# Kernel optimization log

Hardware: AMD Instinct MI355X
Metric: run time of the kernel (lower is better)

## Reference

```python
import jax, jax.numpy as jnp
import numpy as np

EXP_EMBD = 1024
EXP_Q_H = 8
EXP_HEAD_DIM = 256
EXP_KV_H = 1
EXP_KV_DIM = EXP_KV_H * EXP_HEAD_DIM  # 256
EXP_FFN = 4096
B, L, LC = 8, 512, 2048


def setup_inputs() -> dict:
    key = jax.random.key(0)
    ks = jax.random.split(key, 12)
    def w(k, shape):
        fan_in = shape[-1]
        return jax.random.normal(k, shape, jnp.float32) * (fan_in ** -0.5)
    return {
        "x": jax.random.normal(ks[0], (B, L, EXP_EMBD), jnp.float32),
        "text_k": jax.random.normal(ks[1], (B, LC, EXP_KV_DIM), jnp.float32),
        "text_v": jax.random.normal(ks[2], (B, LC, EXP_KV_DIM), jnp.float32),
        "ln1_w": jnp.ones((EXP_EMBD,), jnp.float32),
        "ln2_w": jnp.ones((EXP_EMBD,), jnp.float32),
        "Wq": w(ks[3], (EXP_Q_H * EXP_HEAD_DIM, EXP_EMBD)),
        "Wk": w(ks[4], (EXP_KV_DIM, EXP_KV_DIM)),
        "Wv": w(ks[5], (EXP_KV_DIM, EXP_KV_DIM)),
        "Wo": w(ks[6], (EXP_EMBD, EXP_Q_H * EXP_HEAD_DIM)),
        "Wg": w(ks[7], (EXP_FFN, EXP_EMBD)),
        "Wu": w(ks[8], (EXP_FFN, EXP_EMBD)),
        "Wd": w(ks[9], (EXP_EMBD, EXP_FFN)),
    }


def _rmsnorm(x, w):
    # torch.nn.RMSNorm with eps=None -> eps = finfo(dtype).eps
    eps = jnp.asarray(jnp.finfo(jnp.float32).eps, x.dtype)
    return x * jax.lax.rsqrt(jnp.mean(x * x, axis=-1, keepdims=True) + eps) * w


def _rope(x):
    # x: [B, L, H, D]
    b, l, h, d = x.shape
    d2 = d // 2
    ts = 10000.0 ** (2.0 / d * jnp.arange(d2, dtype=jnp.float32))  # [d2]
    rad = jnp.arange(l, dtype=jnp.float32)[:, None] / ts[None, :]  # [L, d2]
    s = jnp.sin(rad)[None, :, None, :]
    c = jnp.cos(rad)[None, :, None, :]
    x1, x2 = x[..., :d2], x[..., d2:]
    return jnp.concatenate([x1 * c - x2 * s, x2 * c + x1 * s], axis=-1)


def reference(x, text_k, text_v, ln1_w, ln2_w, Wq, Wk, Wv, Wo, Wg, Wu, Wd):
    b, l, _ = x.shape
    lc = text_k.shape[1]
    residual = x
    h = _rmsnorm(x, ln1_w)
    q = _rope((h @ Wq.T).reshape(b, l, EXP_Q_H, EXP_HEAD_DIM))          # [B,L,QH,D]
    k = (text_k @ Wk.T).reshape(b, lc, EXP_KV_H, EXP_HEAD_DIM)          # [B,Lc,KVH,D]
    v = (text_v @ Wv.T).reshape(b, lc, EXP_KV_H, EXP_HEAD_DIM)
    kv_map = (jnp.arange(EXP_Q_H) * EXP_KV_H) // EXP_Q_H                # GQA head map
    kh = jnp.take(k, kv_map, axis=2)                                    # [B,Lc,QH,D]
    vh = jnp.take(v, kv_map, axis=2)
    scale = 1.0 / np.sqrt(EXP_HEAD_DIM).astype(np.float32)
    scores = jnp.einsum('blhd,bchd->bhlc', q, kh) * scale               # [B,QH,L,Lc]
    attn = jax.nn.softmax(scores, axis=-1)
    ctx = jnp.einsum('bhlc,bchd->blhd', attn, vh).reshape(b, l, -1)
    x = ctx @ Wo.T + residual
    residual = x
    h = _rmsnorm(x, ln2_w)
    return (jax.nn.silu(h @ Wg.T) * (h @ Wu.T)) @ Wd.T + residual
```

## Files before the change

kernel.cpp:

```cpp
#include <hip/hip_runtime.h>

typedef __attribute__((ext_vector_type(4))) float f32x4;
typedef __attribute__((ext_vector_type(8))) short s16x8;
typedef __attribute__((ext_vector_type(4))) unsigned short u16x4;

#define B_    8
#define L_    512
#define LC_   2048
#define EMBD  1024

__device__ __forceinline__ float b2f(unsigned short u) {
  unsigned int i = ((unsigned int)u) << 16;
  float f; __builtin_memcpy(&f, &i, 4); return f;
}
__device__ __forceinline__ unsigned short f2b(float f) {
  unsigned int i; __builtin_memcpy(&i, &f, 4);
  unsigned int r = i + 0x7FFFu + ((i >> 16) & 1u);
  return (unsigned short)(r >> 16);
}

#define GLL16(g, l)                                                         \
  __builtin_amdgcn_global_load_lds(                                         \
      (__attribute__((address_space(1))) void*)(g),                         \
      (__attribute__((address_space(3))) void*)(l), 16, 0, 0)

__global__ __launch_bounds__(256) void convert_f32_bf16(
    const float* __restrict__ in, unsigned short* __restrict__ out, int n4) {
  int i = blockIdx.x * 256 + threadIdx.x;
  if (i >= n4) return;
  float4 v = ((const float4*)in)[i];
  u16x4 o = { f2b(v.x), f2b(v.y), f2b(v.z), f2b(v.w) };
  ((u16x4*)out)[i] = o;
}

__global__ __launch_bounds__(256) void rmsnorm_kernel(
    const float* __restrict__ x, const float* __restrict__ w,
    unsigned short* __restrict__ out) {
  int row = blockIdx.x;
  int tid = threadIdx.x;
  float4 v = ((const float4*)(x + (size_t)row * EMBD))[tid];
  float ss = v.x*v.x + v.y*v.y + v.z*v.z + v.w*v.w;
#pragma unroll
  for (int o = 1; o < 64; o <<= 1) ss += __shfl_xor(ss, o);
  __shared__ float red[4];
  if ((tid & 63) == 0) red[tid >> 6] = ss;
  __syncthreads();
  float tot = red[0] + red[1] + red[2] + red[3];
  float rs = rsqrtf(tot * (1.0f / EMBD) + 1.1920928955078125e-07f);
  float4 wv = ((const float4*)w)[tid];
  u16x4 o = { f2b(v.x*rs*wv.x), f2b(v.y*rs*wv.y), f2b(v.z*rs*wv.z), f2b(v.w*rs*wv.w) };
  ((u16x4*)(out + (size_t)row * EMBD))[tid] = o;
}

__global__ __launch_bounds__(256) void rope_kernel(unsigned short* __restrict__ q) {
  int idx = blockIdx.x * 256 + threadIdx.x;
  int i   = idx & 127;
  int h   = (idx >> 7) & 7;
  int row = idx >> 10;
  int l   = row & (L_ - 1);
  size_t base = (size_t)row * 2048 + h * 256 + i;
  float x1 = b2f(q[base]);
  float x2 = b2f(q[base + 128]);
  float ts  = powf(10000.0f, (float)i * (2.0f / 256.0f));
  float rad = (float)l / ts;
  float s, c;
  sincosf(rad, &s, &c);
  q[base]       = f2b(x1 * c - x2 * s);
  q[base + 128] = f2b(x2 * c + x1 * s);
}

__global__ __launch_bounds__(256) void act_kernel(
    const unsigned short* __restrict__ g, const unsigned short* __restrict__ u,
    unsigned short* __restrict__ out, int n8) {
  int i = blockIdx.x * 256 + threadIdx.x;
  if (i >= n8) return;
  s16x8 gv = ((const s16x8*)g)[i];
  s16x8 uv = ((const s16x8*)u)[i];
  s16x8 ov;
#pragma unroll
  for (int j = 0; j < 8; ++j) {
    float gf = b2f((unsigned short)gv[j]);
    float uf = b2f((unsigned short)uv[j]);
    float s  = gf / (1.0f + __expf(-gf));
    ov[j] = (short)f2b(s * uf);
  }
  ((s16x8*)out)[i] = ov;
}

template <int ADD_RES, int OUT_BF16>
__global__ __launch_bounds__(256, 2) void gemm_nt(
    const unsigned short* __restrict__ A, const unsigned short* __restrict__ Bw,
    const float* __restrict__ Res, void* __restrict__ C, int M, int N, int K) {
  __shared__ unsigned short As[128 * 64];
  __shared__ unsigned short Bs[128 * 64];
  const int tid = threadIdx.x;
  const int lane = tid & 63, wid = tid >> 6;
  const int l15 = lane & 15, l4 = lane >> 4;
  const int wr = wid >> 1, wc = wid & 1;
  const int m0 = blockIdx.y * 128, n0 = blockIdx.x * 128;

  const f32x4 fz = {0.f, 0.f, 0.f, 0.f};
  f32x4 acc[4][4];
#pragma unroll
  for (int i = 0; i < 4; ++i)
#pragma unroll
    for (int j = 0; j < 4; ++j) acc[i][j] = fz;

  for (int k0 = 0; k0 < K; k0 += 64) {
    __syncthreads();
#pragma unroll
    for (int i = 0; i < 4; ++i) {
      int Li = i * 4096 + tid * 16;
      int row = Li >> 7;
      int kb = (Li & 127) ^ ((row & 7) << 4);
      GLL16((const char*)(A + (size_t)(m0 + row) * K + k0) + kb, (char*)As + Li);
      GLL16((const char*)(Bw + (size_t)(n0 + row) * K + k0) + kb, (char*)Bs + Li);
    }
    __syncthreads();
#pragma unroll
    for (int kk = 0; kk < 2; ++kk) {
      s16x8 af[4], bfr[4];
#pragma unroll
      for (int mi = 0; mi < 4; ++mi) {
        int row = wr * 64 + mi * 16 + l15;
        int kb = (kk * 64 + l4 * 16) ^ ((row & 7) << 4);
        af[mi] = *(const s16x8*)((const char*)As + row * 128 + kb);
      }
#pragma unroll
      for (int ni = 0; ni < 4; ++ni) {
        int row = wc * 64 + ni * 16 + l15;
        int kb = (kk * 64 + l4 * 16) ^ ((row & 7) << 4);
        bfr[ni] = *(const s16x8*)((const char*)Bs + row * 128 + kb);
      }
#pragma unroll
      for (int mi = 0; mi < 4; ++mi)
#pragma unroll
        for (int ni = 0; ni < 4; ++ni)
          acc[mi][ni] = __builtin_amdgcn_mfma_f32_16x16x32_bf16(
              af[mi], bfr[ni], acc[mi][ni], 0, 0, 0);
    }
  }
#pragma unroll
  for (int mi = 0; mi < 4; ++mi) {
#pragma unroll
    for (int r = 0; r < 4; ++r) {
      int grow = m0 + wr * 64 + mi * 16 + l4 * 4 + r;
      size_t base = (size_t)grow * N + n0 + wc * 64 + l15;
#pragma unroll
      for (int ni = 0; ni < 4; ++ni) {
        float v = acc[mi][ni][r];
        size_t idx = base + ni * 16;
        if (ADD_RES) v += Res[idx];
        if (OUT_BF16) ((unsigned short*)C)[idx] = f2b(v);
        else          ((float*)C)[idx] = v;
      }
    }
  }
}

#define SWZV(d) (((((d) & 7) ^ (((d) >> 3) & 7))) << 4)

__global__ __launch_bounds__(512, 2) void attn_kernel(
    const unsigned short* __restrict__ Q,
    const unsigned short* __restrict__ Kc,
    const unsigned short* __restrict__ Vc,
    unsigned short* __restrict__ Ctx) {
  __shared__ unsigned short Ks[64 * 256];
  __shared__ unsigned short Vt[256 * 64];
  const int tid = threadIdx.x;
  const int lane = tid & 63, wid = tid >> 6;
  const int l15 = lane & 15, g = lane >> 4;
  const int qt = blockIdx.x, h = blockIdx.y, b = blockIdx.z;

  const size_t qrow = (size_t)(b * L_ + qt * 128 + wid * 16 + l15);
  const unsigned short* qp = Q + qrow * 2048 + h * 256;
  s16x8 qf[8];
#pragma unroll
  for (int kc = 0; kc < 8; ++kc) qf[kc] = *(const s16x8*)(qp + kc * 32 + g * 8);

  const f32x4 fz = {0.f, 0.f, 0.f, 0.f};
  f32x4 oacc[16];
#pragma unroll
  for (int i = 0; i < 16; ++i) oacc[i] = fz;
  float m_run = -__builtin_inff(), l_run = 0.f;

  const unsigned short* Kb = Kc + (size_t)b * LC_ * 256;
  const unsigned short* Vb = Vc + (size_t)b * LC_ * 256;

  for (int kt = 0; kt < LC_ / 64; ++kt) {
    __syncthreads();
#pragma unroll
    for (int i = 0; i < 4; ++i) {
      int Li = i * 8192 + tid * 16;
      int row = Li >> 9;
      int kb = (Li & 511) ^ ((row & 7) << 4);
      GLL16((const char*)(Kb + (size_t)(kt * 64 + row) * 256) + kb, (char*)Ks + Li);
    }
#pragma unroll
    for (int p = 0; p < 2; ++p) {
      int id = p * 512 + tid;
      int dgrp = id & 31;
      int kvp = id >> 5;
      int d0 = dgrp * 8, kv0 = kvp * 2;
      const unsigned short* v0p = Vb + (size_t)(kt * 64 + kv0) * 256 + d0;
      s16x8 r0 = *(const s16x8*)v0p;
      s16x8 r1 = *(const s16x8*)(v0p + 256);
#pragma unroll
      for (int j = 0; j < 8; ++j) {
        int d = d0 + j;
        unsigned int val = (unsigned int)(unsigned short)r0[j] |
                           ((unsigned int)(unsigned short)r1[j] << 16);
        *(unsigned int*)((char*)Vt + d * 128 + ((kv0 * 2) ^ SWZV(d))) = val;
      }
    }
    __syncthreads();

    f32x4 sacc[4];
#pragma unroll
    for (int mi = 0; mi < 4; ++mi) sacc[mi] = fz;
#pragma unroll
    for (int mi = 0; mi < 4; ++mi) {
      int row = mi * 16 + l15;
      int swz = (row & 7) << 4;
#pragma unroll
      for (int kc = 0; kc < 8; ++kc) {
        s16x8 kf = *(const s16x8*)((const char*)Ks + row * 512 + ((kc * 64 + g * 16) ^ swz));
        sacc[mi] = __builtin_amdgcn_mfma_f32_16x16x32_bf16(kf, qf[kc], sacc[mi], 0, 0, 0);
      }
    }
    float sv[4][4];
    float mt = -__builtin_inff();
#pragma unroll
    for (int mi = 0; mi < 4; ++mi)
#pragma unroll
      for (int r = 0; r < 4; ++r) {
        float t = sacc[mi][r] * 0.0625f;
        sv[mi][r] = t;
        mt = fmaxf(mt, t);
      }
    mt = fmaxf(mt, __shfl_xor(mt, 16));
    mt = fmaxf(mt, __shfl_xor(mt, 32));
    float mnew = fmaxf(m_run, mt);
    float alpha = __expf(m_run - mnew);
    float rs = 0.f;
#pragma unroll
    for (int mi = 0; mi < 4; ++mi)
#pragma unroll
      for (int r = 0; r < 4; ++r) {
        float p = __expf(sv[mi][r] - mnew);
        sv[mi][r] = p;
        rs += p;
      }
    rs += __shfl_xor(rs, 16);
    rs += __shfl_xor(rs, 32);
    l_run = l_run * alpha + rs;
    m_run = mnew;
    float af4[4];
#pragma unroll
    for (int r = 0; r < 4; ++r) af4[r] = __shfl(alpha, g * 4 + r);
#pragma unroll
    for (int nd = 0; nd < 16; ++nd)
#pragma unroll
      for (int r = 0; r < 4; ++r) oacc[nd][r] *= af4[r];
    unsigned int pk[4][2];
#pragma unroll
    for (int ni = 0; ni < 4; ++ni) {
      pk[ni][0] = (unsigned int)f2b(sv[ni][0]) | ((unsigned int)f2b(sv[ni][1]) << 16);
      pk[ni][1] = (unsigned int)f2b(sv[ni][2]) | ((unsigned int)f2b(sv[ni][3]) << 16);
    }
    int cbase = (g & 1) << 3;
#pragma unroll
    for (int t = 0; t < 2; ++t) {
      unsigned int w[4];
#pragma unroll
      for (int jj = 0; jj < 4; ++jj) {
        int c = cbase + (jj << 1);
        int src = ((c >> 2) << 4) + l15;
        unsigned int ra = __shfl(pk[2 * t][jj & 1], src);
        unsigned int rb = __shfl(pk[2 * t + 1][jj & 1], src);
        w[jj] = (g < 2) ? ra : rb;
      }
      union { unsigned int u[4]; s16x8 v; } cvt;
      cvt.u[0] = w[0]; cvt.u[1] = w[1]; cvt.u[2] = w[2]; cvt.u[3] = w[3];
      s16x8 ap = cvt.v;
#pragma unroll
      for (int nd = 0; nd < 16; ++nd) {
        int d = nd * 16 + l15;
        s16x8 vf = *(const s16x8*)((const char*)Vt + d * 128 + ((t * 64 + g * 16) ^ SWZV(d)));
        oacc[nd] = __builtin_amdgcn_mfma_f32_16x16x32_bf16(ap, vf, oacc[nd], 0, 0, 0);
      }
    }
  }
  float lf[4];
#pragma unroll
  for (int r = 0; r < 4; ++r) lf[r] = 1.0f / __shfl(l_run, g * 4 + r);
  const size_t orow0 = (size_t)(b * L_ + qt * 128 + wid * 16);
#pragma unroll
  for (int r = 0; r < 4; ++r) {
    size_t base = (orow0 + g * 4 + r) * 2048 + h * 256 + l15;
#pragma unroll
    for (int nd = 0; nd < 16; ++nd)
      Ctx[base + nd * 16] = f2b(oacc[nd][r] * lf[r]);
  }
}

extern "C" void kernel_launch(void* const* d_in, const int* in_sizes, int n_in,
                              void* d_out, int out_size, void* d_ws, size_t ws_size,
                              hipStream_t stream) {
  const float* x   = (const float*)d_in[0];
  const float* tk  = (const float*)d_in[1];
  const float* tv  = (const float*)d_in[2];
  const float* ln1 = (const float*)d_in[3];
  const float* ln2 = (const float*)d_in[4];
  const float* Wq  = (const float*)d_in[5];
  const float* Wk  = (const float*)d_in[6];
  const float* Wv  = (const float*)d_in[7];
  const float* Wo  = (const float*)d_in[8];
  const float* Wg  = (const float*)d_in[9];
  const float* Wu  = (const float*)d_in[10];
  const float* Wd  = (const float*)d_in[11];
  float* out = (float*)d_out;
  char* ws = (char*)d_ws;

  unsigned short* tk_bf  = (unsigned short*)(ws + 0);
  unsigned short* tv_bf  = (unsigned short*)(ws + 8388608);
  unsigned short* k_bf   = (unsigned short*)(ws + 16777216);
  unsigned short* v_bf   = (unsigned short*)(ws + 25165824);
  unsigned short* g_bf   = (unsigned short*)(ws + 0);
  unsigned short* q_bf   = (unsigned short*)(ws + 33554432);
  unsigned short* ctx_bf = (unsigned short*)(ws + 50331648);
  unsigned short* u_bf   = (unsigned short*)(ws + 33554432);
  unsigned short* wq_bf  = (unsigned short*)(ws + 67108864);
  unsigned short* wk_bf  = (unsigned short*)(ws + 71303168);
  unsigned short* wv_bf  = (unsigned short*)(ws + 71434240);
  unsigned short* wo_bf  = (unsigned short*)(ws + 71565312);
  unsigned short* wg_bf  = (unsigned short*)(ws + 75759616);
  unsigned short* wu_bf  = (unsigned short*)(ws + 84148224);
  unsigned short* wd_bf  = (unsigned short*)(ws + 92536832);
  unsigned short* h_bf   = (unsigned short*)(ws + 100925440);
  float*          x2     = (float*)(ws + 109314048);

  dim3 blk(256);
  auto cvt = [&](const float* src, unsigned short* dst, int n) {
    convert_f32_bf16<<<dim3(n / 1024), blk, 0, stream>>>(src, dst, n / 4);
  };
  cvt(Wq, wq_bf, 2097152);
  cvt(Wk, wk_bf, 65536);
  cvt(Wv, wv_bf, 65536);
  cvt(Wo, wo_bf, 2097152);
  cvt(Wg, wg_bf, 4194304);
  cvt(Wu, wu_bf, 4194304);
  cvt(Wd, wd_bf, 4194304);
  cvt(tk, tk_bf, 4194304);
  cvt(tv, tv_bf, 4194304);

  rmsnorm_kernel<<<dim3(4096), blk, 0, stream>>>(x, ln1, h_bf);
  gemm_nt<0, 1><<<dim3(16, 32), blk, 0, stream>>>(h_bf, wq_bf, nullptr, q_bf, 4096, 2048, 1024);
  rope_kernel<<<dim3(16384), blk, 0, stream>>>(q_bf);
  gemm_nt<0, 1><<<dim3(2, 128), blk, 0, stream>>>(tk_bf, wk_bf, nullptr, k_bf, 16384, 256, 256);
  gemm_nt<0, 1><<<dim3(2, 128), blk, 0, stream>>>(tv_bf, wv_bf, nullptr, v_bf, 16384, 256, 256);
  attn_kernel<<<dim3(4, 8, 8), dim3(512), 0, stream>>>(q_bf, k_bf, v_bf, ctx_bf);
  gemm_nt<1, 0><<<dim3(8, 32), blk, 0, stream>>>(ctx_bf, wo_bf, x, x2, 4096, 1024, 2048);
  rmsnorm_kernel<<<dim3(4096), blk, 0, stream>>>(x2, ln2, h_bf);
  gemm_nt<0, 1><<<dim3(32, 32), blk, 0, stream>>>(h_bf, wg_bf, nullptr, g_bf, 4096, 4096, 1024);
  gemm_nt<0, 1><<<dim3(32, 32), blk, 0, stream>>>(h_bf, wu_bf, nullptr, u_bf, 4096, 4096, 1024);
  act_kernel<<<dim3(8192), blk, 0, stream>>>(g_bf, u_bf, g_bf, 2097152);
  gemm_nt<1, 0><<<dim3(8, 32), blk, 0, stream>>>(g_bf, wd_bf, x2, out, 4096, 1024, 4096);
}
```

Baseline: 432.9 us.

## Add 256x256 pipelined GEMM for gate/up projections and halve attention block size

Adds a new 512-thread GEMM kernel with 256x256 output tiles, double-buffered LDS staging via global_load_lds, explicit vmcnt waits, barriers and setprio to interleave loads with MFMA, and uses it for the two 4096x4096x1024 FFN projections. Attention blocks shrink from 128 to 64 query rows (256 threads), doubling grid size, with the V-transpose loop reworked to load four rows per thread. The larger GEMM tile cuts global traffic per FLOP but uses 128 KB of LDS and yields only 256 blocks. The smaller attention blocks raise occupancy but reload each K/V tile twice as often.

Result: slower. 442.3 us (+2.2%).

```diff
diff --git a/kernel.cpp b/kernel.cpp
--- a/kernel.cpp
+++ b/kernel.cpp
@@ -23,6 +23,10 @@
   __builtin_amdgcn_global_load_lds(                                         \
       (__attribute__((address_space(1))) void*)(g),                         \
       (__attribute__((address_space(3))) void*)(l), 16, 0, 0)
+
+#define VMCNT6() asm volatile("s_waitcnt vmcnt(6)" ::: "memory")
+#define VMCNT0() asm volatile("s_waitcnt vmcnt(0)" ::: "memory")
+#define LGKM0()  asm volatile("s_waitcnt lgkmcnt(0)" ::: "memory")
 
 __global__ __launch_bounds__(256) void convert_f32_bf16(
     const float* __restrict__ in, unsigned short* __restrict__ out, int n4) {
@@ -158,9 +162,160 @@
   }
 }
 
+__global__ __launch_bounds__(512, 2) void gemm256(
+    const unsigned short* __restrict__ A, const unsigned short* __restrict__ Bw,
+    unsigned short* __restrict__ C, int M, int N, int K) {
+  extern __shared__ char smem[];
+  const int tid = threadIdx.x;
+  const int lane = tid & 63;
+  const int wid = tid >> 6;
+  const int wr = wid >> 2, wc = wid & 3;
+  const int l15 = lane & 15, g = lane >> 4;
+  const int m0 = blockIdx.y * 256, n0 = blockIdx.x * 256;
+  const int T = K >> 6;
+  const int swz = (l15 & 7) << 4;
+
+  auto stage = [&](int t, int mat, int half) {
+    char* dst = smem + mat * 65536 + (t & 1) * 32768 + half * 16384;
+    const unsigned short* src = (mat ? Bw + (size_t)(n0 + half * 128) * K
+                                     : A + (size_t)(m0 + half * 128) * K) + t * 64;
+#pragma unroll
+    for (int i = 0; i < 2; ++i) {
+      int Li = i * 8192 + tid * 16;
+      int row = Li >> 7;
+      int kb = (Li & 127) ^ ((row & 7) << 4);
+      GLL16((const char*)(src + (size_t)row * K) + kb, dst + Li);
+    }
+  };
+
+  const f32x4 fz = {0.f, 0.f, 0.f, 0.f};
+  f32x4 acc[2][2][4][2];
+#pragma unroll
+  for (int ms = 0; ms < 2; ++ms)
+#pragma unroll
+    for (int ns = 0; ns < 2; ++ns)
+#pragma unroll
+      for (int mi = 0; mi < 4; ++mi)
+#pragma unroll
+        for (int ni = 0; ni < 2; ++ni) acc[ms][ns][mi][ni] = fz;
+
+  stage(0, 1, 0); stage(0, 1, 1); stage(0, 0, 0); stage(0, 0, 1);
+  stage(1, 1, 0); stage(1, 1, 1); stage(1, 0, 0);
+  VMCNT6();
+  __builtin_amdgcn_s_barrier();
+
+  for (int t = 0; t < T; ++t) {
+    char* Ab = smem + (t & 1) * 32768 + wr * 16384;
+    char* Bb = smem + 65536 + (t & 1) * 32768 + (wc >> 1) * 16384;
+    const int bn = (wc & 1) * 64;
+    s16x8 a[4][2], b0[2][2], b1[2][2];
+
+#pragma unroll
+    for (int mi = 0; mi < 4; ++mi) {
+      int row = mi * 16 + l15;
+#pragma unroll
+      for (int kk = 0; kk < 2; ++kk)
+        a[mi][kk] = *(const s16x8*)(Ab + row * 128 + ((kk * 64 + g * 16) ^ swz));
+    }
+#pragma unroll
+    for (int ni = 0; ni < 2; ++ni) {
+      int r0 = (bn + ni * 16 + l15) * 128;
+      int r1 = (bn + 32 + ni * 16 + l15) * 128;
+#pragma unroll
+      for (int kk = 0; kk < 2; ++kk) {
+        int ko = (kk * 64 + g * 16) ^ swz;
+        b0[ni][kk] = *(const s16x8*)(Bb + r0 + ko);
+        b1[ni][kk] = *(const s16x8*)(Bb + r1 + ko);
+      }
+    }
+    if (t + 1 < T) stage(t + 1, 0, 1);
+    __builtin_amdgcn_s_barrier();
+    LGKM0();
+    __builtin_amdgcn_sched_barrier(0);
+    __builtin_amdgcn_s_setprio(1);
+#pragma unroll
+    for (int mi = 0; mi < 4; ++mi)
+#pragma unroll
+      for (int ni = 0; ni < 2; ++ni)
+#pragma unroll
+        for (int kk = 0; kk < 2; ++kk)
+          acc[0][0][mi][ni] = __builtin_amdgcn_mfma_f32_16x16x32_bf16(
+              a[mi][kk], b0[ni][kk], acc[0][0][mi][ni], 0, 0, 0);
+    __builtin_amdgcn_s_setprio(0);
+    __builtin_amdgcn_s_barrier();
+
+    if (t + 2 < T) stage(t + 2, 1, 0);
+    __builtin_amdgcn_s_barrier();
+    __builtin_amdgcn_s_setprio(1);
+#pragma unroll
+    for (int mi = 0; mi < 4; ++mi)
+#pragma unroll
+      for (int ni = 0; ni < 2; ++ni)
+#pragma unroll
+        for (int kk = 0; kk < 2; ++kk)
+          acc[0][1][mi][ni] = __builtin_amdgcn_mfma_f32_16x16x32_bf16(
+              a[mi][kk], b1[ni][kk], acc[0][1][mi][ni], 0, 0, 0);
+    __builtin_amdgcn_s_setprio(0);
+    __builtin_amdgcn_s_barrier();
+
+#pragma unroll
+    for (int mi = 0; mi < 4; ++mi) {
+      int row = 64 + mi * 16 + l15;
+#pragma unroll
+      for (int kk = 0; kk < 2; ++kk)
+        a[mi][kk] = *(const s16x8*)(Ab + row * 128 + ((kk * 64 + g * 16) ^ swz));
+    }
+    if (t + 2 < T) stage(t + 2, 1, 1);
+    __builtin_amdgcn_s_barrier();
+    LGKM0();
+    __builtin_amdgcn_sched_barrier(0);
+    __builtin_amdgcn_s_setprio(1);
+#pragma unroll
+    for (int mi = 0; mi < 4; ++mi)
+#pragma unroll
+      for (int ni = 0; ni < 2; ++ni)
+#pragma unroll
+        for (int kk = 0; kk < 2; ++kk)
+          acc[1][0][mi][ni] = __builtin_amdgcn_mfma_f32_16x16x32_bf16(
+              a[mi][kk], b0[ni][kk], acc[1][0][mi][ni], 0, 0, 0);
+    __builtin_amdgcn_s_setprio(0);
+    __builtin_amdgcn_s_barrier();
+
+    if (t + 2 < T) { stage(t + 2, 0, 0); VMCNT6(); }
+    else           { VMCNT0(); }
+    __builtin_amdgcn_s_barrier();
+    __builtin_amdgcn_s_setprio(1);
+#pragma unroll
+    for (int mi = 0; mi < 4; ++mi)
+#pragma unroll
+      for (int ni = 0; ni < 2; ++ni)
+#pragma unroll
+        for (int kk = 0; kk < 2; ++kk)
+          acc[1][1][mi][ni] = __builtin_amdgcn_mfma_f32_16x16x32_bf16(
+              a[mi][kk], b1[ni][kk], acc[1][1][mi][ni], 0, 0, 0);
+    __builtin_amdgcn_s_setprio(0);
+    __builtin_amdgcn_s_barrier();
+  }
+
+#pragma unroll
+  for (int ms = 0; ms < 2; ++ms)
+#pragma unroll
+    for (int mi = 0; mi < 4; ++mi)
+#pragma unroll
+      for (int r = 0; r < 4; ++r) {
+        int grow = m0 + wr * 128 + ms * 64 + mi * 16 + g * 4 + r;
+        size_t base = (size_t)grow * N + n0 + wc * 64;
+#pragma unroll
+        for (int ns = 0; ns < 2; ++ns)
+#pragma unroll
+          for (int ni = 0; ni < 2; ++ni)
+            C[base + ns * 32 + ni * 16 + l15] = f2b(acc[ms][ns][mi][ni][r]);
+      }
+}
+
 #define SWZV(d) (((((d) & 7) ^ (((d) >> 3) & 7))) << 4)
 
-__global__ __launch_bounds__(512, 2) void attn_kernel(
+__global__ __launch_bounds__(256, 2) void attn_kernel(
     const unsigned short* __restrict__ Q,
     const unsigned short* __restrict__ Kc,
     const unsigned short* __restrict__ Vc,
@@ -172,7 +327,7 @@
   const int l15 = lane & 15, g = lane >> 4;
   const int qt = blockIdx.x, h = blockIdx.y, b = blockIdx.z;
 
-  const size_t qrow = (size_t)(b * L_ + qt * 128 + wid * 16 + l15);
+  const size_t qrow = (size_t)(b * L_ + qt * 64 + wid * 16 + l15);
   const unsigned short* qp = Q + qrow * 2048 + h * 256;
   s16x8 qf[8];
 #pragma unroll
@@ -190,27 +345,32 @@
   for (int kt = 0; kt < LC_ / 64; ++kt) {
     __syncthreads();
 #pragma unroll
-    for (int i = 0; i < 4; ++i) {
-      int Li = i * 8192 + tid * 16;
+    for (int i = 0; i < 8; ++i) {
+      int Li = i * 4096 + tid * 16;
       int row = Li >> 9;
       int kb = (Li & 511) ^ ((row & 7) << 4);
       GLL16((const char*)(Kb + (size_t)(kt * 64 + row) * 256) + kb, (char*)Ks + Li);
     }
 #pragma unroll
     for (int p = 0; p < 2; ++p) {
-      int id = p * 512 + tid;
+      int id = p * 256 + tid;
       int dgrp = id & 31;
-      int kvp = id >> 5;
-      int d0 = dgrp * 8, kv0 = kvp * 2;
-      const unsigned short* v0p = Vb + (size_t)(kt * 64 + kv0) * 256 + d0;
-      s16x8 r0 = *(const s16x8*)v0p;
-      s16x8 r1 = *(const s16x8*)(v0p + 256);
+      int kvq = id >> 5;
+      int d0 = dgrp * 8, kv0 = kvq * 4;
+      const unsigned short* vp = Vb + (size_t)(kt * 64 + kv0) * 256 + d0;
+      s16x8 r0 = *(const s16x8*)vp;
+      s16x8 r1 = *(const s16x8*)(vp + 256);
+      s16x8 r2 = *(const s16x8*)(vp + 512);
+      s16x8 r3 = *(const s16x8*)(vp + 768);
 #pragma unroll
       for (int j = 0; j < 8; ++j) {
         int d = d0 + j;
-        unsigned int val = (unsigned int)(unsigned short)r0[j] |
-                           ((unsigned int)(unsigned short)r1[j] << 16);
-        *(unsigned int*)((char*)Vt + d * 128 + ((kv0 * 2) ^ SWZV(d))) = val;
+        uint2 val;
+        val.x = (unsigned int)(unsigned short)r0[j] |
+                ((unsigned int)(unsigned short)r1[j] << 16);
+        val.y = (unsigned int)(unsigned short)r2[j] |
+                ((unsigned int)(unsigned short)r3[j] << 16);
+        *(uint2*)((char*)Vt + d * 128 + ((kvq * 8) ^ SWZV(d))) = val;
       }
     }
     __syncthreads();
@@ -294,7 +454,7 @@
   float lf[4];
 #pragma unroll
   for (int r = 0; r < 4; ++r) lf[r] = 1.0f / __shfl(l_run, g * 4 + r);
-  const size_t orow0 = (size_t)(b * L_ + qt * 128 + wid * 16);
+  const size_t orow0 = (size_t)(b * L_ + qt * 64 + wid * 16);
 #pragma unroll
   for (int r = 0; r < 4; ++r) {
     size_t base = (orow0 + g * 4 + r) * 2048 + h * 256 + l15;
@@ -322,6 +482,9 @@
   float* out = (float*)d_out;
   char* ws = (char*)d_ws;
 
+  (void)hipFuncSetAttribute((const void*)gemm256,
+                            hipFuncAttributeMaxDynamicSharedMemorySize, 131072);
+
   unsigned short* tk_bf  = (unsigned short*)(ws + 0);
   unsigned short* tv_bf  = (unsigned short*)(ws + 8388608);
   unsigned short* k_bf   = (unsigned short*)(ws + 16777216);
@@ -359,11 +522,11 @@
   rope_kernel<<<dim3(16384), blk, 0, stream>>>(q_bf);
   gemm_nt<0, 1><<<dim3(2, 128), blk, 0, stream>>>(tk_bf, wk_bf, nullptr, k_bf, 16384, 256, 256);
   gemm_nt<0, 1><<<dim3(2, 128), blk, 0, stream>>>(tv_bf, wv_bf, nullptr, v_bf, 16384, 256, 256);
-  attn_kernel<<<dim3(4, 8, 8), dim3(512), 0, stream>>>(q_bf, k_bf, v_bf, ctx_bf);
+  attn_kernel<<<dim3(8, 8, 8), dim3(256), 0, stream>>>(q_bf, k_bf, v_bf, ctx_bf);
   gemm_nt<1, 0><<<dim3(8, 32), blk, 0, stream>>>(ctx_bf, wo_bf, x, x2, 4096, 1024, 2048);
   rmsnorm_kernel<<<dim3(4096), blk, 0, stream>>>(x2, ln2, h_bf);
-  gemm_nt<0, 1><<<dim3(32, 32), blk, 0, stream>>>(h_bf, wg_bf, nullptr, g_bf, 4096, 4096, 1024);
-  gemm_nt<0, 1><<<dim3(32, 32), blk, 0, stream>>>(h_bf, wu_bf, nullptr, u_bf, 4096, 4096, 1024);
+  gemm256<<<dim3(16, 16), dim3(512), 131072, stream>>>(h_bf, wg_bf, g_bf, 4096, 4096, 1024);
+  gemm256<<<dim3(16, 16), dim3(512), 131072, stream>>>(h_bf, wu_bf, u_bf, 4096, 4096, 1024);
   act_kernel<<<dim3(8192), blk, 0, stream>>>(g_bf, u_bf, g_bf, 2097152);
   gemm_nt<1, 0><<<dim3(8, 32), blk, 0, stream>>>(g_bf, wd_bf, x2, out, 4096, 1024, 4096);
 }
```
